# Kernel optimization log

Measured on AMD Instinct MI355X. Metric: run time of the kernel, lower is better.

Reference implementation:

```python
import jax, jax.numpy as jnp
import numpy as np
import math

EPS = 1.1920929e-07  # torch.finfo(float32).eps, used by nn.RMSNorm when eps=None
N_HEADS = 16

def _rmsnorm(x, w):
    return x * jax.lax.rsqrt(jnp.mean(x * x, axis=-1, keepdims=True) + EPS) * w

def setup_inputs() -> dict:
    key = jax.random.key(0)
    D, V, FF = 1024, 32000, 2048
    NS, IPS = 4, 8
    B, T = 2, 1024
    ks = jax.random.split(key, 8)
    sd = 0.02
    g = lambda i, shape: jax.random.normal(ks[i], shape, jnp.float32) * sd
    return {
        "tokens": jax.random.randint(ks[0], (B, T), 0, V),
        "embed_w": g(1, (V, D)),
        "qkv_w": g(2, (3 * D, D)),
        "o_w": g(3, (D, D)),
        "gate_w": g(4, (FF, D)),
        "up_w": g(5, (FF, D)),
        "down_w": g(6, (D, FF)),
        "norm1_w": jnp.ones((D,), jnp.float32),
        "norm2_w": jnp.ones((D,), jnp.float32),
        "scale_gamma": jnp.ones((NS, D), jnp.float32),
        "scale_beta": jnp.zeros((NS, D), jnp.float32),
        "iter_scale": jnp.ones((NS, IPS), jnp.float32),
        "norm_w": jnp.ones((D,), jnp.float32),
        "lm_head_w": g(7, (V, D)),
    }

def _block(x, gamma, beta, qkv_w, o_w, gate_w, up_w, down_w, norm1_w, norm2_w):
    B, T, D = x.shape
    hd = D // N_HEADS
    # pre-attn norm + FiLM modulation
    h = _rmsnorm(x, norm1_w) * gamma + beta
    qkv = (h @ qkv_w.T).reshape(B, T, 3, N_HEADS, hd)
    q = jnp.transpose(qkv[:, :, 0], (0, 2, 1, 3))  # [B,H,T,hd]
    k = jnp.transpose(qkv[:, :, 1], (0, 2, 1, 3))
    v = jnp.transpose(qkv[:, :, 2], (0, 2, 1, 3))
    scores = jnp.einsum('bhqd,bhkd->bhqk', q, k) / math.sqrt(hd)
    causal = jnp.tril(jnp.ones((T, T), dtype=bool))
    scores = jnp.where(causal, scores, -jnp.inf)
    attn = jax.nn.softmax(scores, axis=-1)
    out = jnp.einsum('bhqk,bhkd->bhqd', attn, v)
    out = jnp.transpose(out, (0, 2, 1, 3)).reshape(B, T, D)
    x = x + out @ o_w.T
    # pre-FFN norm + FiLM modulation, SwiGLU
    h2 = _rmsnorm(x, norm2_w) * gamma + beta
    x = x + (jax.nn.silu(h2 @ gate_w.T) * (h2 @ up_w.T)) @ down_w.T
    return x

def reference(tokens, embed_w, qkv_w, o_w, gate_w, up_w, down_w, norm1_w,
              norm2_w, scale_gamma, scale_beta, iter_scale, norm_w, lm_head_w):
    NS, IPS = iter_scale.shape
    x = embed_w[tokens].astype(jnp.float32)  # [B,T,D]
    # flatten (scale, iter) schedule to per-virtual-layer params [NS*IPS, ...]
    gammas = jnp.repeat(scale_gamma, IPS, axis=0)
    betas = jnp.repeat(scale_beta, IPS, axis=0)
    iters = iter_scale.reshape(-1)

    @jax.checkpoint
    def step(x, per):
        g, b, s = per
        y = _block(x, g, b, qkv_w, o_w, gate_w, up_w, down_w, norm1_w, norm2_w)
        return x + (y - x) * s, None

    x, _ = jax.lax.scan(step, x, (gammas, betas, iters))
    return _rmsnorm(x, norm_w) @ lm_head_w.T  # [B,T,V]
```

## Files before the change

### kernel.cpp

```cpp
#include <hip/hip_runtime.h>

typedef __bf16 bf16;
typedef __attribute__((ext_vector_type(8))) __bf16 bf16x8;
typedef __attribute__((ext_vector_type(4))) __bf16 bf16x4;
typedef __attribute__((ext_vector_type(4))) float f32x4;

#define MFMA16(a,b,c) __builtin_amdgcn_mfma_f32_16x16x32_bf16((a),(b),(c),0,0,0)

__device__ __forceinline__ void gload16(const void* g, void* l) {
    __builtin_amdgcn_global_load_lds((const __attribute__((address_space(1))) void*)g,
                                     (__attribute__((address_space(3))) void*)l, 16, 0, 0);
}

__device__ __forceinline__ int xcd_swizzle(int orig, int nwg) {
    int q = nwg >> 3, r = nwg & 7;
    int xcd = orig & 7, loc = orig >> 3;
    int base = (xcd < r) ? xcd * (q + 1) : r * (q + 1) + (xcd - r) * q;
    return base + loc;
}


__global__ __launch_bounds__(256) void cvt_kernel(const float* __restrict__ in,
                                                  bf16* __restrict__ out, int n4) {
    int stride = gridDim.x * 256;
    for (int i = blockIdx.x * 256 + threadIdx.x; i < n4; i += stride) {
        float4 v = ((const float4*)in)[i];
        bf16x4 o;
        o[0] = (bf16)v.x; o[1] = (bf16)v.y; o[2] = (bf16)v.z; o[3] = (bf16)v.w;
        ((bf16x4*)out)[i] = o;
    }
}

__global__ __launch_bounds__(256) void embed_kernel(const int* __restrict__ tok,
                                                    const float* __restrict__ ew,
                                                    float* __restrict__ X) {
    int m = blockIdx.x;
    int t = tok[m];
    ((float4*)(X + (size_t)m * 1024))[threadIdx.x] =
        ((const float4*)(ew + (size_t)t * 1024))[threadIdx.x];
}

template <bool FILM>
__global__ __launch_bounds__(256) void rmsnorm_kernel(const float* __restrict__ X,
                                                      const float* __restrict__ w,
                                                      const float* __restrict__ gamma,
                                                      const float* __restrict__ beta,
                                                      bf16* __restrict__ H) {
    int m = blockIdx.x, t = threadIdx.x;
    float4 xv = ((const float4*)(X + (size_t)m * 1024))[t];
    float ss = xv.x * xv.x + xv.y * xv.y + xv.z * xv.z + xv.w * xv.w;
#pragma unroll
    for (int off = 1; off < 64; off <<= 1) ss += __shfl_xor(ss, off);
    __shared__ float red[4];
    if ((t & 63) == 0) red[t >> 6] = ss;
    __syncthreads();
    float tot = red[0] + red[1] + red[2] + red[3];
    float sc = rsqrtf(tot * (1.0f / 1024.0f) + 1.1920929e-07f);
    float4 wv = ((const float4*)w)[t];
    float r0 = xv.x * sc * wv.x, r1 = xv.y * sc * wv.y;
    float r2 = xv.z * sc * wv.z, r3 = xv.w * sc * wv.w;
    if (FILM) {
        float4 gv = ((const float4*)gamma)[t];
        float4 bv = ((const float4*)beta)[t];
        r0 = r0 * gv.x + bv.x; r1 = r1 * gv.y + bv.y;
        r2 = r2 * gv.z + bv.z; r3 = r3 * gv.w + bv.w;
    }
    bf16x4 o;
    o[0] = (bf16)r0; o[1] = (bf16)r1; o[2] = (bf16)r2; o[3] = (bf16)r3;
    ((bf16x4*)(H + (size_t)m * 1024))[t] = o;
}


__global__ __launch_bounds__(256) void vtrans_kernel(const bf16* __restrict__ QKV,
                                                     bf16* __restrict__ VT) {
    const int tt = blockIdx.x, bh = blockIdx.y;
    const int b = bh >> 4, h = bh & 15;
    __shared__ __align__(16) bf16 Ls[64 * 72];
    const int tid = threadIdx.x;
#pragma unroll
    for (int i = 0; i < 2; ++i) {
        int cid = tid + 256 * i;
        int r = cid >> 3, c8 = (cid & 7) * 8;
        *(bf16x8*)(Ls + r * 72 + c8) =
            *(const bf16x8*)(QKV + (size_t)(b * 1024 + tt * 64 + r) * 3072 + 2048 + h * 64 + c8);
    }
    __syncthreads();
#pragma unroll
    for (int i = 0; i < 2; ++i) {
        int cid = tid + 256 * i;
        int d = cid >> 3, k8 = (cid & 7) * 8;
        bf16x8 v;
#pragma unroll
        for (int j = 0; j < 8; ++j) v[j] = Ls[(k8 + j) * 72 + d];
        *(bf16x8*)(VT + (size_t)bh * 65536 + (size_t)d * 1024 + tt * 64 + k8) = v;
    }
}


template <int MT, int MODE, bool BNF>
__global__ __launch_bounds__(256, 2) void gemm_bt(const bf16* __restrict__ A,
                                                  const bf16* __restrict__ B,
                                                  int GN, int GM,
                                                  int N, int K,
                                                  bf16* __restrict__ Cb, float* __restrict__ Cf,
                                                  const float* __restrict__ Xin,
                                                  const float* __restrict__ Xin2,
                                                  float* __restrict__ Xout,
                                                  const float* __restrict__ sptr) {
    constexpr int BM = 32 * MT;
    __shared__ __align__(16) bf16 As[BM * 64];
    __shared__ __align__(16) bf16 Bs[128 * 64];
    const int wg = xcd_swizzle(blockIdx.x, GN * GM);
    int bn, bm;
    if (BNF) { bm = wg / GN; bn = wg - bm * GN; }
    else     { bn = wg / GM; bm = wg - bn * GM; }
    const int tid = threadIdx.x, lane = tid & 63, w = tid >> 6;
    const int wr = w >> 1, wc = w & 1, lr = lane & 15, lg = lane >> 4;
    const bf16* Ab = A + (size_t)bm * BM * K;
    const bf16* Bb = B + (size_t)bn * 128 * K;

    f32x4 acc[MT][4];
#pragma unroll
    for (int i = 0; i < MT; ++i)
#pragma unroll
        for (int j = 0; j < 4; ++j) acc[i][j] = (f32x4){0.f, 0.f, 0.f, 0.f};

    for (int kt = 0; kt < K; kt += 64) {
        __syncthreads();
#pragma unroll
        for (int i = 0; i < MT; ++i) {
            int cw = i * 256 + w * 64;
            int cid = cw + lane;
            gload16(Ab + (size_t)(cid >> 3) * K + kt + (cid & 7) * 8, As + cw * 8);
        }
#pragma unroll
        for (int i = 0; i < 4; ++i) {
            int cw = i * 256 + w * 64;
            int cid = cw + lane;
            gload16(Bb + (size_t)(cid >> 3) * K + kt + (cid & 7) * 8, Bs + cw * 8);
        }
        __syncthreads();
#pragma unroll
        for (int kk = 0; kk < 64; kk += 32) {
            bf16x8 af[MT], bfr[4];
#pragma unroll
            for (int mi = 0; mi < MT; ++mi)
                af[mi] = *(const bf16x8*)(As + (wr * (16 * MT) + mi * 16 + lr) * 64 + kk + lg * 8);
#pragma unroll
            for (int ni = 0; ni < 4; ++ni)
                bfr[ni] = *(const bf16x8*)(Bs + (wc * 64 + ni * 16 + lr) * 64 + kk + lg * 8);
#pragma unroll
            for (int mi = 0; mi < MT; ++mi)
#pragma unroll
                for (int ni = 0; ni < 4; ++ni)
                    acc[mi][ni] = MFMA16(af[mi], bfr[ni], acc[mi][ni]);
        }
    }

    float s1 = (MODE == 2) ? sptr[0] : 0.f;
#pragma unroll
    for (int mi = 0; mi < MT; ++mi) {
#pragma unroll
        for (int ni = 0; ni < 4; ++ni) {
#pragma unroll
            for (int j = 0; j < 4; ++j) {
                int row = bm * BM + wr * (16 * MT) + mi * 16 + lg * 4 + j;
                int col = bn * 128 + wc * 64 + ni * 16 + lr;
                size_t idx = (size_t)row * N + col;
                float v = acc[mi][ni][j];
                if (MODE == 0) Cb[idx] = (bf16)v;
                else if (MODE == 1) Xout[idx] = Xin[idx] + v;
                else if (MODE == 2) Xout[idx] = Xin[idx] + s1 * (Xin2[idx] - Xin[idx] + v);
                else Cf[idx] = v;
            }
        }
    }
}


__global__ __launch_bounds__(256, 2) void gemm_gateup(const bf16* __restrict__ A,
                                                      const bf16* __restrict__ Bg,
                                                      const bf16* __restrict__ Bu,
                                                      bf16* __restrict__ FF) {
    const int K = 1024, N = 2048;
    __shared__ __align__(16) bf16 As[128 * 64];
    __shared__ __align__(16) bf16 Gs[128 * 64];
    __shared__ __align__(16) bf16 Us[128 * 64];
    const int wg = xcd_swizzle(blockIdx.x, 256);
    const int bn = wg >> 4, bm = wg & 15;
    const int tid = threadIdx.x, lane = tid & 63, w = tid >> 6;
    const int wr = w >> 1, wc = w & 1, lr = lane & 15, lg = lane >> 4;
    const bf16* Ab = A + (size_t)bm * 128 * K;
    const bf16* Gb = Bg + (size_t)bn * 128 * K;
    const bf16* Ub = Bu + (size_t)bn * 128 * K;

    f32x4 ag[4][4], au[4][4];
#pragma unroll
    for (int i = 0; i < 4; ++i)
#pragma unroll
        for (int j = 0; j < 4; ++j) {
            ag[i][j] = (f32x4){0.f, 0.f, 0.f, 0.f};
            au[i][j] = (f32x4){0.f, 0.f, 0.f, 0.f};
        }

    for (int kt = 0; kt < K; kt += 64) {
        __syncthreads();
#pragma unroll
        for (int i = 0; i < 4; ++i) {
            int cw = i * 256 + w * 64;
            int cid = cw + lane;
            size_t ro = (size_t)(cid >> 3) * K + kt + (cid & 7) * 8;
            gload16(Ab + ro, As + cw * 8);
            gload16(Gb + ro, Gs + cw * 8);
            gload16(Ub + ro, Us + cw * 8);
        }
        __syncthreads();
#pragma unroll
        for (int kk = 0; kk < 64; kk += 32) {
            bf16x8 af[4], gf[4], uf[4];
#pragma unroll
            for (int mi = 0; mi < 4; ++mi)
                af[mi] = *(const bf16x8*)(As + (wr * 64 + mi * 16 + lr) * 64 + kk + lg * 8);
#pragma unroll
            for (int ni = 0; ni < 4; ++ni) {
                gf[ni] = *(const bf16x8*)(Gs + (wc * 64 + ni * 16 + lr) * 64 + kk + lg * 8);
                uf[ni] = *(const bf16x8*)(Us + (wc * 64 + ni * 16 + lr) * 64 + kk + lg * 8);
            }
#pragma unroll
            for (int mi = 0; mi < 4; ++mi)
#pragma unroll
                for (int ni = 0; ni < 4; ++ni) {
                    ag[mi][ni] = MFMA16(af[mi], gf[ni], ag[mi][ni]);
                    au[mi][ni] = MFMA16(af[mi], uf[ni], au[mi][ni]);
                }
        }
    }

#pragma unroll
    for (int mi = 0; mi < 4; ++mi) {
#pragma unroll
        for (int ni = 0; ni < 4; ++ni) {
#pragma unroll
            for (int j = 0; j < 4; ++j) {
                int row = bm * 128 + wr * 64 + mi * 16 + lg * 4 + j;
                int col = bn * 128 + wc * 64 + ni * 16 + lr;
                float g = ag[mi][ni][j], u = au[mi][ni][j];
                float sg = g / (1.0f + __expf(-g));
                FF[(size_t)row * N + col] = (bf16)(sg * u);
            }
        }
    }
}


__global__ __launch_bounds__(256) void attn_kernel(const bf16* __restrict__ QKV,
                                                   const bf16* __restrict__ VTg,
                                                   bf16* __restrict__ AO) {
    const int qt = blockIdx.x, bh = blockIdx.y;
    const int b = bh >> 4, h = bh & 15;
    const int tid = threadIdx.x;
    const int w = tid >> 6, lane = tid & 63;
    const int lr = lane & 15, lg = lane >> 4;

    __shared__ __align__(16) bf16 Ks[64 * 72];
    __shared__ __align__(16) bf16 Vt[64 * 72];
    __shared__ __align__(16) bf16 Ps[4 * 16 * 72];
    bf16* Pw = Ps + w * 16 * 72;

    const int qrow = b * 1024 + qt * 64 + w * 16 + lr;
    const bf16* qptr = QKV + (size_t)qrow * 3072 + h * 64;
    const bf16* vt_src = VTg + (size_t)bh * 65536;
    bf16x8 qf0 = *(const bf16x8*)(qptr + lg * 8);
    bf16x8 qf1 = *(const bf16x8*)(qptr + 32 + lg * 8);

    f32x4 o[4];
#pragma unroll
    for (int i = 0; i < 4; ++i) o[i] = (f32x4){0.f, 0.f, 0.f, 0.f};
    float m_run = -1e30f, l_run = 0.f;
    const int gq = qt * 64 + w * 16 + lr;

    for (int kt = 0; kt <= qt; ++kt) {
        __syncthreads();
#pragma unroll
        for (int i = 0; i < 2; ++i) {
            int cid = tid + 256 * i;
            int r = cid >> 3, c8 = (cid & 7) * 8;
            const bf16* kvrow = QKV + (size_t)(b * 1024 + kt * 64 + r) * 3072 + h * 64;
            *(bf16x8*)(Ks + r * 72 + c8) = *(const bf16x8*)(kvrow + 1024 + c8);
            *(bf16x8*)(Vt + r * 72 + c8) =
                *(const bf16x8*)(vt_src + (size_t)r * 1024 + kt * 64 + c8);
        }
        __syncthreads();

        f32x4 st[4];
#pragma unroll
        for (int i = 0; i < 4; ++i) st[i] = (f32x4){0.f, 0.f, 0.f, 0.f};
        __builtin_amdgcn_s_setprio(1);
#pragma unroll
        for (int ki = 0; ki < 4; ++ki) {
            bf16x8 kf0 = *(const bf16x8*)(Ks + (ki * 16 + lr) * 72 + lg * 8);
            bf16x8 kf1 = *(const bf16x8*)(Ks + (ki * 16 + lr) * 72 + 32 + lg * 8);
            st[ki] = MFMA16(kf0, qf0, st[ki]);
            st[ki] = MFMA16(kf1, qf1, st[ki]);
        }
        __builtin_amdgcn_s_setprio(0);
        bool diag = (kt == qt);
        float pm = -1e30f;
#pragma unroll
        for (int ki = 0; ki < 4; ++ki) {
#pragma unroll
            for (int j = 0; j < 4; ++j) {
                float sv = st[ki][j] * 0.125f;
                if (diag) {
                    int gk = kt * 64 + ki * 16 + lg * 4 + j;
                    if (gk > gq) sv = -1e30f;
                }
                st[ki][j] = sv;
                pm = fmaxf(pm, sv);
            }
        }
        pm = fmaxf(pm, __shfl_xor(pm, 16));
        pm = fmaxf(pm, __shfl_xor(pm, 32));
        float m_new = fmaxf(m_run, pm);
        float alpha = __expf(m_run - m_new);
        float rs = 0.f;
#pragma unroll
        for (int ki = 0; ki < 4; ++ki) {
            bf16x4 pb;
#pragma unroll
            for (int j = 0; j < 4; ++j) {
                float pv = __expf(st[ki][j] - m_new);
                rs += pv;
                pb[j] = (bf16)pv;
            }
            *(bf16x4*)(Pw + lr * 72 + ki * 16 + lg * 4) = pb;
        }
        rs += __shfl_xor(rs, 16);
        rs += __shfl_xor(rs, 32);
        l_run = l_run * alpha + rs;
        m_run = m_new;
#pragma unroll
        for (int di = 0; di < 4; ++di) o[di] *= alpha;
        __builtin_amdgcn_s_setprio(1);
#pragma unroll
        for (int dk = 0; dk < 2; ++dk) {
            bf16x8 pf = *(const bf16x8*)(Pw + lr * 72 + dk * 32 + lg * 8);
#pragma unroll
            for (int di = 0; di < 4; ++di) {
                bf16x8 vf = *(const bf16x8*)(Vt + (di * 16 + lr) * 72 + dk * 32 + lg * 8);
                o[di] = MFMA16(vf, pf, o[di]);
            }
        }
        __builtin_amdgcn_s_setprio(0);
    }
    float inv = 1.0f / l_run;
    bf16* optr = AO + (size_t)qrow * 1024 + h * 64;
#pragma unroll
    for (int di = 0; di < 4; ++di) {
        bf16x4 ov;
#pragma unroll
        for (int j = 0; j < 4; ++j) ov[j] = (bf16)(o[di][j] * inv);
        *(bf16x4*)(optr + di * 16 + lg * 4) = ov;
    }
}


extern "C" void kernel_launch(void* const* d_in, const int* in_sizes, int n_in,
                              void* d_out, int out_size, void* d_ws, size_t ws_size,
                              hipStream_t stream) {
    const int* tokens = (const int*)d_in[0];
    const float* embed_w = (const float*)d_in[1];
    const float* qkv_w = (const float*)d_in[2];
    const float* o_w = (const float*)d_in[3];
    const float* gate_w = (const float*)d_in[4];
    const float* up_w = (const float*)d_in[5];
    const float* down_w = (const float*)d_in[6];
    const float* norm1_w = (const float*)d_in[7];
    const float* norm2_w = (const float*)d_in[8];
    const float* scale_gamma = (const float*)d_in[9];
    const float* scale_beta = (const float*)d_in[10];
    const float* iter_scale = (const float*)d_in[11];
    const float* norm_w = (const float*)d_in[12];
    const float* lm_head_w = (const float*)d_in[13];

    char* p = (char*)d_ws;
    auto alloc = [&](size_t nbytes) -> char* {
        char* r = p;
        p += (nbytes + 255) & ~(size_t)255;
        return r;
    };
    bf16* WQKV = (bf16*)alloc(3072ull * 1024 * 2);
    bf16* WO   = (bf16*)alloc(1024ull * 1024 * 2);
    bf16* WG   = (bf16*)alloc(2048ull * 1024 * 2);
    bf16* WU   = (bf16*)alloc(2048ull * 1024 * 2);
    bf16* WD   = (bf16*)alloc(1024ull * 2048 * 2);
    bf16* WLM  = (bf16*)alloc(32000ull * 1024 * 2);
    float* X   = (float*)alloc(2048ull * 1024 * 4);
    float* X1  = (float*)alloc(2048ull * 1024 * 4);
    bf16* H    = (bf16*)alloc(2048ull * 1024 * 2);
    bf16* QKVb = (bf16*)alloc(2048ull * 3072 * 2);
    bf16* VT   = (bf16*)alloc(2048ull * 1024 * 2);
    bf16* AO   = (bf16*)alloc(2048ull * 1024 * 2);
    bf16* FF   = (bf16*)alloc(2048ull * 2048 * 2);

    cvt_kernel<<<1024, 256, 0, stream>>>(qkv_w, WQKV, 3072 * 1024 / 4);
    cvt_kernel<<<1024, 256, 0, stream>>>(o_w, WO, 1024 * 1024 / 4);
    cvt_kernel<<<1024, 256, 0, stream>>>(gate_w, WG, 2048 * 1024 / 4);
    cvt_kernel<<<1024, 256, 0, stream>>>(up_w, WU, 2048 * 1024 / 4);
    cvt_kernel<<<1024, 256, 0, stream>>>(down_w, WD, 1024 * 2048 / 4);
    cvt_kernel<<<2048, 256, 0, stream>>>(lm_head_w, WLM, 32000 * 1024 / 4);
    embed_kernel<<<2048, 256, 0, stream>>>(tokens, embed_w, X);

    for (int l = 0; l < 32; ++l) {
        const float* gm = scale_gamma + (size_t)(l >> 3) * 1024;
        const float* bt = scale_beta + (size_t)(l >> 3) * 1024;
        rmsnorm_kernel<true><<<2048, 256, 0, stream>>>(X, norm1_w, gm, bt, H);
        gemm_bt<4, 0, false><<<24 * 16, 256, 0, stream>>>(H, WQKV, 24, 16, 3072, 1024,
                                                          QKVb, nullptr, nullptr, nullptr, nullptr, nullptr);
        vtrans_kernel<<<dim3(16, 32), 256, 0, stream>>>(QKVb, VT);
        attn_kernel<<<dim3(16, 32), 256, 0, stream>>>(QKVb, VT, AO);
        gemm_bt<2, 1, true><<<8 * 32, 256, 0, stream>>>(AO, WO, 8, 32, 1024, 1024,
                                                        nullptr, nullptr, X, nullptr, X1, nullptr);
        rmsnorm_kernel<true><<<2048, 256, 0, stream>>>(X1, norm2_w, gm, bt, H);
        gemm_gateup<<<256, 256, 0, stream>>>(H, WG, WU, FF);
        gemm_bt<2, 2, true><<<8 * 32, 256, 0, stream>>>(FF, WD, 8, 32, 1024, 2048,
                                                        nullptr, nullptr, X, X1, X, iter_scale + l);
    }
    rmsnorm_kernel<false><<<2048, 256, 0, stream>>>(X, norm_w, nullptr, nullptr, H);
    gemm_bt<4, 3, false><<<250 * 16, 256, 0, stream>>>(H, WLM, 250, 16, 32000, 1024,
                                                       nullptr, (float*)d_out, nullptr, nullptr, nullptr, nullptr);
}
```

Baseline: 5.057 ms.

## Double-buffer LDS tiles in GEMMs and halve gate/up M tile

Adds two-stage LDS double buffering to gemm_bt and gemm_gateup so the next K-tile's global-to-LDS loads are issued before computing on the current tile, with one barrier per iteration instead of two. The gate/up kernel also shrinks its M tile from 128 to 64 rows, doubling the grid to 512 workgroups for better CU coverage. This doubles LDS per block, which may limit occupancy, and the smaller gate/up tile reduces reuse of the weight tiles.

```diff
diff --git a/kernel.cpp b/kernel.cpp
--- a/kernel.cpp
+++ b/kernel.cpp
@@ -108,8 +108,8 @@
                                                   float* __restrict__ Xout,
                                                   const float* __restrict__ sptr) {
     constexpr int BM = 32 * MT;
-    __shared__ __align__(16) bf16 As[BM * 64];
-    __shared__ __align__(16) bf16 Bs[128 * 64];
+    __shared__ __align__(16) bf16 As[2][BM * 64];
+    __shared__ __align__(16) bf16 Bs[2][128 * 64];
     const int wg = xcd_swizzle(blockIdx.x, GN * GM);
     int bn, bm;
     if (BNF) { bm = wg / GN; bn = wg - bm * GN; }
@@ -125,37 +125,48 @@
 #pragma unroll
         for (int j = 0; j < 4; ++j) acc[i][j] = (f32x4){0.f, 0.f, 0.f, 0.f};
 
+#define STAGE_AB(buf, ktv)                                                        \
+    do {                                                                          \
+        _Pragma("unroll")                                                         \
+        for (int i = 0; i < MT; ++i) {                                            \
+            int cw = i * 256 + w * 64; int cid = cw + lane;                       \
+            gload16(Ab + (size_t)(cid >> 3) * K + (ktv) + (cid & 7) * 8,          \
+                    As[buf] + cw * 8);                                            \
+        }                                                                         \
+        _Pragma("unroll")                                                         \
+        for (int i = 0; i < 4; ++i) {                                             \
+            int cw = i * 256 + w * 64; int cid = cw + lane;                       \
+            gload16(Bb + (size_t)(cid >> 3) * K + (ktv) + (cid & 7) * 8,          \
+                    Bs[buf] + cw * 8);                                            \
+        }                                                                         \
+    } while (0)
+
+    STAGE_AB(0, 0);
+    __syncthreads();
+    int cur = 0;
     for (int kt = 0; kt < K; kt += 64) {
-        __syncthreads();
-#pragma unroll
-        for (int i = 0; i < MT; ++i) {
-            int cw = i * 256 + w * 64;
-            int cid = cw + lane;
-            gload16(Ab + (size_t)(cid >> 3) * K + kt + (cid & 7) * 8, As + cw * 8);
-        }
-#pragma unroll
-        for (int i = 0; i < 4; ++i) {
-            int cw = i * 256 + w * 64;
-            int cid = cw + lane;
-            gload16(Bb + (size_t)(cid >> 3) * K + kt + (cid & 7) * 8, Bs + cw * 8);
-        }
-        __syncthreads();
+        if (kt + 64 < K) STAGE_AB(cur ^ 1, kt + 64);
+        const bf16* Asc = As[cur];
+        const bf16* Bsc = Bs[cur];
 #pragma unroll
         for (int kk = 0; kk < 64; kk += 32) {
             bf16x8 af[MT], bfr[4];
 #pragma unroll
             for (int mi = 0; mi < MT; ++mi)
-                af[mi] = *(const bf16x8*)(As + (wr * (16 * MT) + mi * 16 + lr) * 64 + kk + lg * 8);
+                af[mi] = *(const bf16x8*)(Asc + (wr * (16 * MT) + mi * 16 + lr) * 64 + kk + lg * 8);
 #pragma unroll
             for (int ni = 0; ni < 4; ++ni)
-                bfr[ni] = *(const bf16x8*)(Bs + (wc * 64 + ni * 16 + lr) * 64 + kk + lg * 8);
+                bfr[ni] = *(const bf16x8*)(Bsc + (wc * 64 + ni * 16 + lr) * 64 + kk + lg * 8);
 #pragma unroll
             for (int mi = 0; mi < MT; ++mi)
 #pragma unroll
                 for (int ni = 0; ni < 4; ++ni)
                     acc[mi][ni] = MFMA16(af[mi], bfr[ni], acc[mi][ni]);
         }
-    }
+        __syncthreads();
+        cur ^= 1;
+    }
+#undef STAGE_AB
 
     float s1 = (MODE == 2) ? sptr[0] : 0.f;
 #pragma unroll
@@ -183,66 +194,82 @@
                                                       const bf16* __restrict__ Bu,
                                                       bf16* __restrict__ FF) {
     const int K = 1024, N = 2048;
-    __shared__ __align__(16) bf16 As[128 * 64];
-    __shared__ __align__(16) bf16 Gs[128 * 64];
-    __shared__ __align__(16) bf16 Us[128 * 64];
-    const int wg = xcd_swizzle(blockIdx.x, 256);
-    const int bn = wg >> 4, bm = wg & 15;
+    __shared__ __align__(16) bf16 As[2][64 * 64];
+    __shared__ __align__(16) bf16 Gs[2][128 * 64];
+    __shared__ __align__(16) bf16 Us[2][128 * 64];
+    const int wg = xcd_swizzle(blockIdx.x, 512);
+    const int bn = wg >> 5, bm = wg & 31;
     const int tid = threadIdx.x, lane = tid & 63, w = tid >> 6;
     const int wr = w >> 1, wc = w & 1, lr = lane & 15, lg = lane >> 4;
-    const bf16* Ab = A + (size_t)bm * 128 * K;
+    const bf16* Ab = A + (size_t)bm * 64 * K;
     const bf16* Gb = Bg + (size_t)bn * 128 * K;
     const bf16* Ub = Bu + (size_t)bn * 128 * K;
 
-    f32x4 ag[4][4], au[4][4];
-#pragma unroll
-    for (int i = 0; i < 4; ++i)
+    f32x4 ag[2][4], au[2][4];
+#pragma unroll
+    for (int i = 0; i < 2; ++i)
 #pragma unroll
         for (int j = 0; j < 4; ++j) {
             ag[i][j] = (f32x4){0.f, 0.f, 0.f, 0.f};
             au[i][j] = (f32x4){0.f, 0.f, 0.f, 0.f};
         }
 
+#define STAGE_GU(buf, ktv)                                                        \
+    do {                                                                          \
+        _Pragma("unroll")                                                         \
+        for (int i = 0; i < 2; ++i) {                                             \
+            int cw = i * 256 + w * 64; int cid = cw + lane;                       \
+            gload16(Ab + (size_t)(cid >> 3) * K + (ktv) + (cid & 7) * 8,          \
+                    As[buf] + cw * 8);                                            \
+        }                                                                         \
+        _Pragma("unroll")                                                         \
+        for (int i = 0; i < 4; ++i) {                                             \
+            int cw = i * 256 + w * 64; int cid = cw + lane;                       \
+            size_t ro = (size_t)(cid >> 3) * K + (ktv) + (cid & 7) * 8;           \
+            gload16(Gb + ro, Gs[buf] + cw * 8);                                   \
+            gload16(Ub + ro, Us[buf] + cw * 8);                                   \
+        }                                                                         \
+    } while (0)
+
+    STAGE_GU(0, 0);
+    __syncthreads();
+    int cur = 0;
     for (int kt = 0; kt < K; kt += 64) {
-        __syncthreads();
-#pragma unroll
-        for (int i = 0; i < 4; ++i) {
-            int cw = i * 256 + w * 64;
-            int cid = cw + lane;
-            size_t ro = (size_t)(cid >> 3) * K + kt + (cid & 7) * 8;
-            gload16(Ab + ro, As + cw * 8);
-            gload16(Gb + ro, Gs + cw * 8);
-            gload16(Ub + ro, Us + cw * 8);
-        }
-        __syncthreads();
+        if (kt + 64 < K) STAGE_GU(cur ^ 1, kt + 64);
+        const bf16* Asc = As[cur];
+        const bf16* Gsc = Gs[cur];
+        const bf16* Usc = Us[cur];
 #pragma unroll
         for (int kk = 0; kk < 64; kk += 32) {
-            bf16x8 af[4], gf[4], uf[4];
-#pragma unroll
-            for (int mi = 0; mi < 4; ++mi)
-                af[mi] = *(const bf16x8*)(As + (wr * 64 + mi * 16 + lr) * 64 + kk + lg * 8);
+            bf16x8 af[2], gf[4], uf[4];
+#pragma unroll
+            for (int mi = 0; mi < 2; ++mi)
+                af[mi] = *(const bf16x8*)(Asc + (wr * 32 + mi * 16 + lr) * 64 + kk + lg * 8);
 #pragma unroll
             for (int ni = 0; ni < 4; ++ni) {
-                gf[ni] = *(const bf16x8*)(Gs + (wc * 64 + ni * 16 + lr) * 64 + kk + lg * 8);
-                uf[ni] = *(const bf16x8*)(Us + (wc * 64 + ni * 16 + lr) * 64 + kk + lg * 8);
-            }
-#pragma unroll
-            for (int mi = 0; mi < 4; ++mi)
+                gf[ni] = *(const bf16x8*)(Gsc + (wc * 64 + ni * 16 + lr) * 64 + kk + lg * 8);
+                uf[ni] = *(const bf16x8*)(Usc + (wc * 64 + ni * 16 + lr) * 64 + kk + lg * 8);
+            }
+#pragma unroll
+            for (int mi = 0; mi < 2; ++mi)
 #pragma unroll
                 for (int ni = 0; ni < 4; ++ni) {
                     ag[mi][ni] = MFMA16(af[mi], gf[ni], ag[mi][ni]);
                     au[mi][ni] = MFMA16(af[mi], uf[ni], au[mi][ni]);
                 }
         }
-    }
-
-#pragma unroll
-    for (int mi = 0; mi < 4; ++mi) {
+        __syncthreads();
+        cur ^= 1;
+    }
+#undef STAGE_GU
+
+#pragma unroll
+    for (int mi = 0; mi < 2; ++mi) {
 #pragma unroll
         for (int ni = 0; ni < 4; ++ni) {
 #pragma unroll
             for (int j = 0; j < 4; ++j) {
-                int row = bm * 128 + wr * 64 + mi * 16 + lg * 4 + j;
+                int row = bm * 64 + wr * 32 + mi * 16 + lg * 4 + j;
                 int col = bn * 128 + wc * 64 + ni * 16 + lr;
                 float g = ag[mi][ni][j], u = au[mi][ni][j];
                 float sg = g / (1.0f + __expf(-g));
@@ -422,7 +449,7 @@
         gemm_bt<2, 1, true><<<8 * 32, 256, 0, stream>>>(AO, WO, 8, 32, 1024, 1024,
                                                         nullptr, nullptr, X, nullptr, X1, nullptr);
         rmsnorm_kernel<true><<<2048, 256, 0, stream>>>(X1, norm2_w, gm, bt, H);
-        gemm_gateup<<<256, 256, 0, stream>>>(H, WG, WU, FF);
+        gemm_gateup<<<512, 256, 0, stream>>>(H, WG, WU, FF);
         gemm_bt<2, 2, true><<<8 * 32, 256, 0, stream>>>(FF, WD, 8, 32, 1024, 2048,
                                                         nullptr, nullptr, X, X1, X, iter_scale + l);
     }
```

Result: no change. 5.083 ms (+0.5%).
